# Kernel tuning notes

Measured on AMD Instinct MI355X. Metric: run time of the kernel, lower is better.

The kernel has to match this reference:

```python
import jax, jax.numpy as jnp
import numpy as np

B, S, D, H = 512, 256, 2, 256


def _lstm_cell(x, h, c, W_ih, W_hh, b_ih, b_hh):
    # PyTorch gate order: i, f, g, o
    gates = x @ W_ih.T + b_ih + h @ W_hh.T + b_hh
    i, f, g, o = jnp.split(gates, 4, axis=-1)
    c_new = jax.nn.sigmoid(f) * c + jax.nn.sigmoid(i) * jnp.tanh(g)
    h_new = jax.nn.sigmoid(o) * jnp.tanh(c_new)
    return h_new, c_new


def setup_inputs() -> dict:
    key = jax.random.key(0)
    ks = jax.random.split(key, 9)
    bound = 1.0 / np.sqrt(H)
    u = lambda k, shp: jax.random.uniform(k, shp, jnp.float32, -bound, bound)
    return {
        "inputs": jax.random.normal(ks[0], (B, S, D), jnp.float32),
        "enc_W_ih": u(ks[1], (4 * H, D)),
        "enc_W_hh": u(ks[2], (4 * H, H)),
        "enc_b_ih": u(ks[3], (4 * H,)),
        "enc_b_hh": u(ks[4], (4 * H,)),
        "dec_W_ih": u(ks[5], (4 * H, H)),
        "dec_W_hh": u(ks[6], (4 * H, H)),
        "dec_b_ih": u(ks[7], (4 * H,)),
        "dec_b_hh": u(ks[8], (4 * H,)),
    }


def reference(inputs, enc_W_ih, enc_W_hh, enc_b_ih, enc_b_hh,
              dec_W_ih, dec_W_hh, dec_b_ih, dec_b_hh):
    bsz, seq_len, _ = inputs.shape
    hid = enc_W_hh.shape[1]

    # ---- encoder LSTM (batch_first), h0 = c0 = 0 ----
    h0 = jnp.zeros((bsz, hid), inputs.dtype)
    c0 = jnp.zeros((bsz, hid), inputs.dtype)

    def enc_step(carry, x_t):
        h, c = carry
        h, c = _lstm_cell(x_t, h, c, enc_W_ih, enc_W_hh, enc_b_ih, enc_b_hh)
        return (h, c), h

    (h_last, c_last), enc_out_t = jax.lax.scan(enc_step, (h0, c0), inputs.transpose(1, 0, 2))
    enc_out = enc_out_t.transpose(1, 0, 2)  # [B, S, H]

    key = jax.random.key(42)
    keys = jax.random.split(key, seq_len)
    dec_in0 = jnp.zeros((bsz, hid), inputs.dtype)
    mask0 = jnp.zeros((bsz, seq_len), dtype=bool)
    rows = jnp.arange(bsz)

    def dec_step(carry, k):
        dec_in, h, c, mask = carry
        h, c = _lstm_cell(dec_in, h, c, dec_W_ih, dec_W_hh, dec_b_ih, dec_b_hh)
        scores = jnp.einsum('bsh,bh->bs', enc_out, h)          # bmm attention
        scores = jnp.where(mask, -jnp.inf, scores)             # mask visited
        idx = jax.random.categorical(k, scores, axis=1)        # multinomial(softmax)
        mask = mask.at[rows, idx].set(True)
        dec_in = jnp.take_along_axis(enc_out, idx[:, None, None], axis=1)[:, 0, :]
        return (dec_in, h, c, mask), idx

    _, indices_t = jax.lax.scan(dec_step, (dec_in0, h_last, c_last, mask0), keys)
    return indices_t.T  # [B, S] int
```

## Files before the change

### kernel.cpp

```cpp
#include <hip/hip_runtime.h>
#include <cstdint>
#include <cstddef>


typedef float v4f __attribute__((ext_vector_type(4)));
typedef unsigned long long u64;

#define WS_HX_OFF     0u
#define WS_AMX_OFF    (1u << 20)
#define WS_SYNC_BYTES 0x110000u
#define WS_ENCW4_OFF  (2u << 20)
#define WS_DECWI4_OFF (3u << 20)
#define WS_DECWH4_OFF (4u << 20)
#define WS_ENCK4_OFF  (5u << 20)
#define WS_NEEDED     ((size_t)(5u << 20) + (size_t)512 * 64 * 256 * 16)

__device__ __forceinline__ unsigned rotl32(unsigned x, int r) {
  return (x << r) | (x >> (32 - r));
}
__device__ __forceinline__ float sigm(float x) { return 1.f / (1.f + expf(-x)); }

__device__ __forceinline__ u64 pk(unsigned tag, unsigned payload) {
  return ((u64)tag << 32) | (u64)payload;
}
__device__ __forceinline__ unsigned spinrd(u64* p, unsigned tag) {
  u64 v = atomicAdd(p, 0ull);
  while ((unsigned)(v >> 32) != tag) {
    __builtin_amdgcn_s_sleep(2);
    v = atomicAdd(p, 0ull);
  }
  return (unsigned)v;
}

__device__ __forceinline__ void tf2(unsigned k0, unsigned k1,
                                    unsigned& x0, unsigned& x1) {
  const unsigned k2 = k0 ^ k1 ^ 0x1BD11BDAu;
  x0 += k0; x1 += k1;
  x0 += x1; x1 = rotl32(x1, 13); x1 ^= x0;
  x0 += x1; x1 = rotl32(x1, 15); x1 ^= x0;
  x0 += x1; x1 = rotl32(x1, 26); x1 ^= x0;
  x0 += x1; x1 = rotl32(x1,  6); x1 ^= x0;
  x0 += k1; x1 += k2 + 1u;
  x0 += x1; x1 = rotl32(x1, 17); x1 ^= x0;
  x0 += x1; x1 = rotl32(x1, 29); x1 ^= x0;
  x0 += x1; x1 = rotl32(x1, 16); x1 ^= x0;
  x0 += x1; x1 = rotl32(x1, 24); x1 ^= x0;
  x0 += k2; x1 += k0 + 2u;
  x0 += x1; x1 = rotl32(x1, 13); x1 ^= x0;
  x0 += x1; x1 = rotl32(x1, 15); x1 ^= x0;
  x0 += x1; x1 = rotl32(x1, 26); x1 ^= x0;
  x0 += x1; x1 = rotl32(x1,  6); x1 ^= x0;
  x0 += k0; x1 += k1 + 3u;
  x0 += x1; x1 = rotl32(x1, 17); x1 ^= x0;
  x0 += x1; x1 = rotl32(x1, 29); x1 ^= x0;
  x0 += x1; x1 = rotl32(x1, 16); x1 ^= x0;
  x0 += x1; x1 = rotl32(x1, 24); x1 ^= x0;
  x0 += k1; x1 += k2 + 4u;
  x0 += x1; x1 = rotl32(x1, 13); x1 ^= x0;
  x0 += x1; x1 = rotl32(x1, 15); x1 ^= x0;
  x0 += x1; x1 = rotl32(x1, 26); x1 ^= x0;
  x0 += x1; x1 = rotl32(x1,  6); x1 ^= x0;
  x0 += k2; x1 += k0 + 5u;
}

__global__ void repack_k(const float* __restrict__ eWh,
                         const float* __restrict__ dWi,
                         const float* __restrict__ dWh,
                         float* __restrict__ ws) {
  float* encW4 = (float*)((char*)ws + WS_ENCW4_OFF);
  float* decWi4 = (float*)((char*)ws + WS_DECWI4_OFF);
  float* decWh4 = (float*)((char*)ws + WS_DECWH4_OFF);
  const int n = blockIdx.x * blockDim.x + threadIdx.x;
  if (n >= 65536) return;
  const int k = n >> 8, u = n & 255;
#pragma unroll
  for (int g = 0; g < 4; ++g) {
    const int src = ((g << 8) + u) * 256 + k;
    const int dst = (n << 2) + g;
    encW4[dst] = eWh[src];
    decWi4[dst] = dWi[src];
    decWh4[dst] = dWh[src];
  }
}

__global__ void __launch_bounds__(1024)
ptrnet_kernel(const float* __restrict__ inp,
              const float* __restrict__ eWi,
              const float* __restrict__ eBi, const float* __restrict__ eBh,
              const float* __restrict__ dBi, const float* __restrict__ dBh,
              int* __restrict__ out,
              float* __restrict__ ws) {
  const int tid  = threadIdx.x;
  const int wave = tid >> 6, l = tid & 63;
  const int kq   = wave >> 2;
  const int uw   = wave & 3;
  const int uP   = (uw << 6) | l;
  const int k4b  = kq << 4;
  const int bA   = tid >> 8;
  const int uA   = tid & 255;

  const int g    = blockIdx.x & 127;
  const int H    = blockIdx.x >> 7;
  const int b0   = g << 2;
  const int bG   = b0 + bA;
  const int ubase = H << 7;
  const int pbase = ubase ^ 128;
  const int sbase = H << 7;

  const v4f* encW4  = (const v4f*)((char*)ws + WS_ENCW4_OFF);
  const v4f* decWi4 = (const v4f*)((char*)ws + WS_DECWI4_OFF);
  const v4f* decWh4 = (const v4f*)((char*)ws + WS_DECWH4_OFF);
  v4f* encK4 = (v4f*)((char*)ws + WS_ENCK4_OFF);

  u64* hxAll  = (u64*)((char*)ws + WS_HX_OFF);
  u64* hxMe   = hxAll + (size_t)g * 1024 + (size_t)H * 512;
  u64* hxYo   = hxAll + (size_t)g * 1024 + (size_t)(1 - H) * 512;
  u64* amxAll = (u64*)((char*)ws + WS_AMX_OFF);
  u64* amxMe  = amxAll + (size_t)g * 16 + (size_t)H * 8;
  u64* amxYo  = amxAll + (size_t)g * 16 + (size_t)(1 - H) * 8;

  __shared__ __align__(16) float hsF[2][1024];
  __shared__ __align__(16) v4f dinV[256];
  __shared__ __align__(16) v4f red[17][256];
  __shared__ unsigned char maskC[4][128];
  __shared__ float partV[4][2];
  __shared__ int   partI[4][2];
  __shared__ float oVs[4]; __shared__ int oIs[4];
  __shared__ float eVs[4]; __shared__ int eIs[4];

  const float ebi_ = eBi[uA] + eBh[uA];
  const float ebf_ = eBi[256 + uA] + eBh[256 + uA];
  const float ebg_ = eBi[512 + uA] + eBh[512 + uA];
  const float ebo_ = eBi[768 + uA] + eBh[768 + uA];
  const float wxi0 = eWi[2 * uA], wxi1 = eWi[2 * uA + 1];
  const float wxf0 = eWi[2 * (256 + uA)], wxf1 = eWi[2 * (256 + uA) + 1];
  const float wxg0 = eWi[2 * (512 + uA)], wxg1 = eWi[2 * (512 + uA) + 1];
  const float wxo0 = eWi[2 * (768 + uA)], wxo1 = eWi[2 * (768 + uA) + 1];

  hsF[0][tid] = 0.f;
  __syncthreads();

  float c = 0.f;
  int p = 0;

  for (int t = 0; t < 256; ++t) {
    v4f a0 = (v4f)0.f, a1 = (v4f)0.f, a2 = (v4f)0.f, a3 = (v4f)0.f;
    const v4f* Wp = encW4 + uP;
    const v4f* hq = (const v4f*)&hsF[p][0];
#pragma unroll 2
    for (int kk = 0; kk < 16; ++kk) {
      const int k4 = k4b + kk;
      const v4f w0 = Wp[(k4 * 4 + 0) << 8];
      const v4f w1 = Wp[(k4 * 4 + 1) << 8];
      const v4f w2 = Wp[(k4 * 4 + 2) << 8];
      const v4f w3 = Wp[(k4 * 4 + 3) << 8];
      const v4f h0 = hq[k4];
      const v4f h1 = hq[64 + k4];
      const v4f h2 = hq[128 + k4];
      const v4f h3 = hq[192 + k4];
      a0 += w0 * h0.x + w1 * h0.y + w2 * h0.z + w3 * h0.w;
      a1 += w0 * h1.x + w1 * h1.y + w2 * h1.z + w3 * h1.w;
      a2 += w0 * h2.x + w1 * h2.y + w2 * h2.z + w3 * h2.w;
      a3 += w0 * h3.x + w1 * h3.y + w2 * h3.z + w3 * h3.w;
    }
    red[(kq << 2) | 0][uP] = a0;
    red[(kq << 2) | 1][uP] = a1;
    red[(kq << 2) | 2][uP] = a2;
    red[(kq << 2) | 3][uP] = a3;
    __syncthreads();
    const v4f gv = red[bA][uA] + red[4 + bA][uA] + red[8 + bA][uA] + red[12 + bA][uA];
    const float2 xv = *(const float2*)(inp + (((bG) << 8) + t) * 2);
    const float ai = gv.x + ebi_ + wxi0 * xv.x + wxi1 * xv.y;
    const float af = gv.y + ebf_ + wxf0 * xv.x + wxf1 * xv.y;
    const float ag = gv.z + ebg_ + wxg0 * xv.x + wxg1 * xv.y;
    const float ao = gv.w + ebo_ + wxo0 * xv.x + wxo1 * xv.y;
    const float iv = sigm(ai), fv = sigm(af), gva = tanhf(ag), ov = sigm(ao);
    c = fv * c + iv * gva;
    const float hn = ov * tanhf(c);
    hsF[p ^ 1][(bA << 8) | uA] = hn;
    ((float*)encK4)[(((bG << 6) + (uA >> 2)) << 10) + (t << 2) + (uA & 3)] = hn;
    __syncthreads();
    p ^= 1;
  }

  float* creg = (float*)&red[0][0];
  creg[(bA << 8) | uA] = c;
  const int isP2 = tid < 512;
  const int bD = tid >> 7;
  const int uL = tid & 127;
  const int uD = ubase | uL;
  __syncthreads();
  float cD = 0.f, dbi2 = 0.f, dbf2 = 0.f, dbg2 = 0.f, dbo2 = 0.f;
  if (isP2) {
    cD = creg[(bD << 8) | uD];
    dbi2 = dBi[uD] + dBh[uD];
    dbf2 = dBi[256 + uD] + dBh[256 + uD];
    dbg2 = dBi[512 + uD] + dBh[512 + uD];
    dbo2 = dBi[768 + uD] + dBh[768 + uD];
  }
  const int aw  = wave - 8;
  const int bAt = aw >> 1;
  const int sL  = ((aw & 1) << 6) | l;
  const int sG  = sbase | sL;
  const int bGt = b0 + bAt;
  if (wave >= 8) maskC[bAt][sL] = 0;
  const int kqD  = wave >> 1;
  const int k4bD = kqD << 4;
  const int uPD  = ubase | ((wave & 1) << 6) | l;
  const float NEG_INF = __int_as_float((int)0xff800000);
  __syncthreads();

  {
    v4f a0 = (v4f)0.f, a1 = (v4f)0.f, a2 = (v4f)0.f, a3 = (v4f)0.f;
    const v4f* Wh = decWh4 + uP;
    const v4f* hq = (const v4f*)&hsF[p][0];
#pragma unroll 2
    for (int kk = 0; kk < 16; ++kk) {
      const int k4 = k4b + kk;
      const v4f w0 = Wh[(k4 * 4 + 0) << 8];
      const v4f w1 = Wh[(k4 * 4 + 1) << 8];
      const v4f w2 = Wh[(k4 * 4 + 2) << 8];
      const v4f w3 = Wh[(k4 * 4 + 3) << 8];
      const v4f h0 = hq[k4];
      const v4f h1 = hq[64 + k4];
      const v4f h2 = hq[128 + k4];
      const v4f h3 = hq[192 + k4];
      a0 += w0 * h0.x + w1 * h0.y + w2 * h0.z + w3 * h0.w;
      a1 += w0 * h1.x + w1 * h1.y + w2 * h1.z + w3 * h1.w;
      a2 += w0 * h2.x + w1 * h2.y + w2 * h2.z + w3 * h2.w;
      a3 += w0 * h3.x + w1 * h3.y + w2 * h3.z + w3 * h3.w;
    }
    red[(kq << 2) | 0][uP] = a0;
    red[(kq << 2) | 1][uP] = a1;
    red[(kq << 2) | 2][uP] = a2;
    red[(kq << 2) | 3][uP] = a3;
    __syncthreads();
    if (isP2) {
      const v4f gv = red[bD][uD] + red[4 + bD][uD] + red[8 + bD][uD] + red[12 + bD][uD];
      const float iv = sigm(gv.x + dbi2), fv = sigm(gv.y + dbf2);
      const float gva = tanhf(gv.z + dbg2), ov = sigm(gv.w + dbo2);
      cD = fv * cD + iv * gva;
      const float hn = ov * tanhf(cD);
      hsF[p ^ 1][(bD << 8) | uD] = hn;
      atomicExch(&hxMe[(bD << 7) | uL], pk(0xA5000000u, __float_as_uint(hn)));
      const unsigned pw = spinrd(&hxYo[(bD << 7) | uL], 0xA5000000u);
      hsF[p ^ 1][(bD << 8) | pbase | uL] = __uint_as_float(pw);
    }
    __syncthreads();
    p ^= 1;
  }

#define WINNER(B, WI) { float _wv = oVs[B]; int _wi = oIs[B];                 \
    const float _ev = eVs[B]; const int _ei = eIs[B];                         \
    if (_ev > _wv || (_ev == _wv && _ei < _wi)) { _wi = _ei; }                \
    WI = _wi; }

  for (int t = 0; t < 256; ++t) {
    const unsigned tagA = 0xA5000001u + 2u * (unsigned)t;
    const unsigned tagH = 0xA5000002u + 2u * (unsigned)t;
    const v4f* hq = (const v4f*)&hsF[p][0];

    if (wave < 8) {
      v4f a0 = (v4f)0.f, a1 = (v4f)0.f, a2 = (v4f)0.f, a3 = (v4f)0.f;
      const v4f* Wh = decWh4 + uPD;
#pragma unroll 2
      for (int kk = 0; kk < 16; ++kk) {
        const int k4 = k4bD + kk;
        const v4f w0 = Wh[(k4 * 4 + 0) << 8];
        const v4f w1 = Wh[(k4 * 4 + 1) << 8];
        const v4f w2 = Wh[(k4 * 4 + 2) << 8];
        const v4f w3 = Wh[(k4 * 4 + 3) << 8];
        const v4f h0 = hq[k4];
        const v4f h1 = hq[64 + k4];
        const v4f h2 = hq[128 + k4];
        const v4f h3 = hq[192 + k4];
        a0 += w0 * h0.x + w1 * h0.y + w2 * h0.z + w3 * h0.w;
        a1 += w0 * h1.x + w1 * h1.y + w2 * h1.z + w3 * h1.w;
        a2 += w0 * h2.x + w1 * h2.y + w2 * h2.z + w3 * h2.w;
        a3 += w0 * h3.x + w1 * h3.y + w2 * h3.z + w3 * h3.w;
      }
      red[(kqD << 2) | 0][uPD] = a0;
      red[(kqD << 2) | 1][uPD] = a1;
      red[(kqD << 2) | 2][uPD] = a2;
      red[(kqD << 2) | 3][uPD] = a3;
    } else {
      const int masked = maskC[bAt][sL];
      float sc = 0.f;
      if (!masked) {
        const v4f* E = encK4 + (bGt << 14) + sG;
        const v4f* hq2 = hq + (bAt << 6);
#pragma unroll 4
        for (int k4 = 0; k4 < 64; ++k4) {
          const v4f ev = E[k4 << 8];
          const v4f hv = hq2[k4];
          sc += ev.x * hv.x + ev.y * hv.y + ev.z * hv.z + ev.w * hv.w;
        }
      }
      unsigned bits;
      {
        unsigned kk0 = 0u, kk1 = (unsigned)t;
        tf2(0u, 42u, kk0, kk1);
        unsigned y0 = 0u, y1 = (unsigned)((bGt << 8) + sG);
        tf2(kk0, kk1, y0, y1);
        bits = y0 ^ y1;
      }
      const float fr = __uint_as_float((bits >> 9) | 0x3f800000u) - 1.0f;
      const float uu = (fr > 0.f) ? fr : 1.17549435e-38f;
      const float gum = -logf(-logf(uu));
      float bv = masked ? NEG_INF : (sc + gum);
      int bi = sG;
#pragma unroll
      for (int off = 32; off; off >>= 1) {
        const float ov2 = __shfl_xor(bv, off, 64);
        const int oi2 = __shfl_xor(bi, off, 64);
        if (ov2 > bv || (ov2 == bv && oi2 < bi)) { bv = ov2; bi = oi2; }
      }
      if (l == 0) { partV[bAt][aw & 1] = bv; partI[bAt][aw & 1] = bi; }
    }
    __syncthreads();

    if (tid < 4) {
      float v0 = partV[tid][0]; int i0 = partI[tid][0];
      const float v1 = partV[tid][1];
      if (v1 > v0) { v0 = v1; i0 = partI[tid][1]; }
      oVs[tid] = v0; oIs[tid] = i0;
      atomicExch(&amxMe[tid * 2 + 0], pk(tagA, __float_as_uint(v0)));
      atomicExch(&amxMe[tid * 2 + 1], pk(tagA, (unsigned)i0));
    }
    if (tid >= 64 && tid < 72) {
      const int j = tid - 64;
      const unsigned pw = spinrd(&amxYo[j], tagA);
      if (j & 1) eIs[j >> 1] = (int)pw;
      else       eVs[j >> 1] = __uint_as_float(pw);
    }
    __syncthreads();

    if (wave >= 8) {
      int wi; WINNER(bAt, wi);
      if (sG == wi) maskC[bAt][sL] = 1;
    }
    if (H == 0 && tid < 4) {
      int wi; WINNER(tid, wi);
      out[((b0 + tid) << 8) + t] = wi;
    }
    if (tid < 256) {
      const int bb = tid >> 6, k4s = tid & 63;
      int wi; WINNER(bb, wi);
      dinV[tid] = encK4[((((b0 + bb) << 6) | k4s) << 8) + wi];
    }
    __syncthreads();

    if (t == 255) break;

    if (wave < 8) {
      v4f a0 = red[(kqD << 2) | 0][uPD];
      v4f a1 = red[(kqD << 2) | 1][uPD];
      v4f a2 = red[(kqD << 2) | 2][uPD];
      v4f a3 = red[(kqD << 2) | 3][uPD];
      const v4f* Wi = decWi4 + uPD;
#pragma unroll 2
      for (int kk = 0; kk < 16; ++kk) {
        const int k4 = k4bD + kk;
        const v4f w0 = Wi[(k4 * 4 + 0) << 8];
        const v4f w1 = Wi[(k4 * 4 + 1) << 8];
        const v4f w2 = Wi[(k4 * 4 + 2) << 8];
        const v4f w3 = Wi[(k4 * 4 + 3) << 8];
        const v4f d0 = dinV[k4];
        const v4f d1 = dinV[64 + k4];
        const v4f d2 = dinV[128 + k4];
        const v4f d3 = dinV[192 + k4];
        a0 += w0 * d0.x + w1 * d0.y + w2 * d0.z + w3 * d0.w;
        a1 += w0 * d1.x + w1 * d1.y + w2 * d1.z + w3 * d1.w;
        a2 += w0 * d2.x + w1 * d2.y + w2 * d2.z + w3 * d2.w;
        a3 += w0 * d3.x + w1 * d3.y + w2 * d3.z + w3 * d3.w;
      }
      red[(kqD << 2) | 0][uPD] = a0;
      red[(kqD << 2) | 1][uPD] = a1;
      red[(kqD << 2) | 2][uPD] = a2;
      red[(kqD << 2) | 3][uPD] = a3;
    }
    __syncthreads();

    if (isP2) {
      const v4f gv = red[bD][uD] + red[4 + bD][uD] + red[8 + bD][uD] + red[12 + bD][uD];
      const float iv = sigm(gv.x + dbi2), fv = sigm(gv.y + dbf2);
      const float gva = tanhf(gv.z + dbg2), ov = sigm(gv.w + dbo2);
      cD = fv * cD + iv * gva;
      const float hn = ov * tanhf(cD);
      hsF[p ^ 1][(bD << 8) | uD] = hn;
      atomicExch(&hxMe[(bD << 7) | uL], pk(tagH, __float_as_uint(hn)));
      const unsigned pw = spinrd(&hxYo[(bD << 7) | uL], tagH);
      hsF[p ^ 1][(bD << 8) | pbase | uL] = __uint_as_float(pw);
    }
    __syncthreads();
    p ^= 1;
  }
#undef WINNER
}

extern "C" void kernel_launch(void* const* d_in, const int* in_sizes, int n_in,
                              void* d_out, int out_size, void* d_ws, size_t ws_size,
                              hipStream_t stream) {
  (void)in_sizes; (void)n_in; (void)out_size;
  if (ws_size < WS_NEEDED) return;

  const float* inp = (const float*)d_in[0];
  const float* eWi = (const float*)d_in[1];
  const float* eWh = (const float*)d_in[2];
  const float* eBi = (const float*)d_in[3];
  const float* eBh = (const float*)d_in[4];
  const float* dWi = (const float*)d_in[5];
  const float* dWh = (const float*)d_in[6];
  const float* dBi = (const float*)d_in[7];
  const float* dBh = (const float*)d_in[8];
  int* out = (int*)d_out;
  float* wsf = (float*)d_ws;

  hipMemsetAsync((char*)d_ws + WS_HX_OFF, 0, WS_SYNC_BYTES, stream);
  hipLaunchKernelGGL(repack_k, dim3(256), dim3(256), 0, stream, eWh, dWi, dWh, wsf);
  hipLaunchKernelGGL(ptrnet_kernel, dim3(256), dim3(1024), 0, stream,
                     inp, eWi, eBi, eBh, dBi, dBh, out, wsf);
}
```

Before: 9.274 ms.

## Split encoder LSTM gate matvec across block pair with cross-block exchange

Each block pair previously computed the full encoder recurrence redundantly. Now each block of the pair handles two of the four gates (repacked as v2f weights), halving per-block weight reads. Gate partial sums and new hidden halves are exchanged with the partner block through global-memory tagged atomics and a spin flag every timestep. This adds two cross-block synchronisations per step on the serial encoder path.

```diff
diff --git a/kernel.cpp b/kernel.cpp
--- a/kernel.cpp
+++ b/kernel.cpp
@@ -4,16 +4,19 @@
 
 
 typedef float v4f __attribute__((ext_vector_type(4)));
+typedef float v2f __attribute__((ext_vector_type(2)));
 typedef unsigned long long u64;
 
-#define WS_HX_OFF     0u
-#define WS_AMX_OFF    (1u << 20)
-#define WS_SYNC_BYTES 0x110000u
-#define WS_ENCW4_OFF  (2u << 20)
-#define WS_DECWI4_OFF (3u << 20)
-#define WS_DECWH4_OFF (4u << 20)
-#define WS_ENCK4_OFF  (5u << 20)
-#define WS_NEEDED     ((size_t)(5u << 20) + (size_t)512 * 64 * 256 * 16)
+#define WS_HX_OFF     0x000000u
+#define WS_GX_OFF     0x100000u
+#define WS_AMX_OFF    0x200000u
+#define WS_GFLAG_OFF  0x204000u
+#define WS_SYNC_BYTES 0x205000u
+#define WS_ENCW2_OFF  0x300000u
+#define WS_DECWI4_OFF 0x400000u
+#define WS_DECWH4_OFF 0x500000u
+#define WS_ENCK4_OFF  0x600000u
+#define WS_NEEDED     ((size_t)WS_ENCK4_OFF + (size_t)512 * 64 * 256 * 16)
 
 __device__ __forceinline__ unsigned rotl32(unsigned x, int r) {
   return (x << r) | (x >> (32 - r));
@@ -67,7 +70,7 @@
                          const float* __restrict__ dWi,
                          const float* __restrict__ dWh,
                          float* __restrict__ ws) {
-  float* encW4 = (float*)((char*)ws + WS_ENCW4_OFF);
+  float* encW2 = (float*)((char*)ws + WS_ENCW2_OFF);
   float* decWi4 = (float*)((char*)ws + WS_DECWI4_OFF);
   float* decWh4 = (float*)((char*)ws + WS_DECWH4_OFF);
   const int n = blockIdx.x * blockDim.x + threadIdx.x;
@@ -76,10 +79,9 @@
 #pragma unroll
   for (int g = 0; g < 4; ++g) {
     const int src = ((g << 8) + u) * 256 + k;
-    const int dst = (n << 2) + g;
-    encW4[dst] = eWh[src];
-    decWi4[dst] = dWi[src];
-    decWh4[dst] = dWh[src];
+    decWi4[(n << 2) + g] = dWi[src];
+    decWh4[(n << 2) + g] = dWh[src];
+    encW2[(((g >> 1) << 16) + n) * 2 + (g & 1)] = eWh[src];
   }
 }
 
@@ -96,18 +98,21 @@
   const int uw   = wave & 3;
   const int uP   = (uw << 6) | l;
   const int k4b  = kq << 4;
-  const int bA   = tid >> 8;
-  const int uA   = tid & 255;
 
   const int g    = blockIdx.x & 127;
   const int H    = blockIdx.x >> 7;
   const int b0   = g << 2;
-  const int bG   = b0 + bA;
   const int ubase = H << 7;
   const int pbase = ubase ^ 128;
   const int sbase = H << 7;
 
-  const v4f* encW4  = (const v4f*)((char*)ws + WS_ENCW4_OFF);
+  const int isP2 = tid < 512;
+  const int bD = tid >> 7;
+  const int uL = tid & 127;
+  const int uD = ubase | uL;
+  const int bGD = b0 + bD;
+
+  const v2f* encW2o = (const v2f*)((char*)ws + WS_ENCW2_OFF) + (H << 16);
   const v4f* decWi4 = (const v4f*)((char*)ws + WS_DECWI4_OFF);
   const v4f* decWh4 = (const v4f*)((char*)ws + WS_DECWH4_OFF);
   v4f* encK4 = (v4f*)((char*)ws + WS_ENCK4_OFF);
@@ -115,9 +120,15 @@
   u64* hxAll  = (u64*)((char*)ws + WS_HX_OFF);
   u64* hxMe   = hxAll + (size_t)g * 1024 + (size_t)H * 512;
   u64* hxYo   = hxAll + (size_t)g * 1024 + (size_t)(1 - H) * 512;
+  u64* gxAll  = (u64*)((char*)ws + WS_GX_OFF);
+  u64* gxMe   = gxAll + (size_t)g * 1024 + (size_t)H * 512;
+  u64* gxYo   = gxAll + (size_t)g * 1024 + (size_t)(1 - H) * 512;
   u64* amxAll = (u64*)((char*)ws + WS_AMX_OFF);
   u64* amxMe  = amxAll + (size_t)g * 16 + (size_t)H * 8;
   u64* amxYo  = amxAll + (size_t)g * 16 + (size_t)(1 - H) * 8;
+  u64* gfAll  = (u64*)((char*)ws + WS_GFLAG_OFF);
+  u64* gflagMe = gfAll + (size_t)g * 2 + (size_t)H;
+  u64* gflagYo = gfAll + (size_t)g * 2 + (size_t)(1 - H);
 
   __shared__ __align__(16) float hsF[2][1024];
   __shared__ __align__(16) v4f dinV[256];
@@ -127,72 +138,100 @@
   __shared__ int   partI[4][2];
   __shared__ float oVs[4]; __shared__ int oIs[4];
   __shared__ float eVs[4]; __shared__ int eIs[4];
-
-  const float ebi_ = eBi[uA] + eBh[uA];
-  const float ebf_ = eBi[256 + uA] + eBh[256 + uA];
-  const float ebg_ = eBi[512 + uA] + eBh[512 + uA];
-  const float ebo_ = eBi[768 + uA] + eBh[768 + uA];
-  const float wxi0 = eWi[2 * uA], wxi1 = eWi[2 * uA + 1];
-  const float wxf0 = eWi[2 * (256 + uA)], wxf1 = eWi[2 * (256 + uA) + 1];
-  const float wxg0 = eWi[2 * (512 + uA)], wxg1 = eWi[2 * (512 + uA) + 1];
-  const float wxo0 = eWi[2 * (768 + uA)], wxo1 = eWi[2 * (768 + uA) + 1];
+  v2f* red2 = (v2f*)&red[0][0];
+
+  const int uB = isP2 ? uD : 0;
+  const float ebi_ = eBi[uB] + eBh[uB];
+  const float ebf_ = eBi[256 + uB] + eBh[256 + uB];
+  const float ebg_ = eBi[512 + uB] + eBh[512 + uB];
+  const float ebo_ = eBi[768 + uB] + eBh[768 + uB];
+  const float wxi0 = eWi[2 * uB], wxi1 = eWi[2 * uB + 1];
+  const float wxf0 = eWi[2 * (256 + uB)], wxf1 = eWi[2 * (256 + uB) + 1];
+  const float wxg0 = eWi[2 * (512 + uB)], wxg1 = eWi[2 * (512 + uB) + 1];
+  const float wxo0 = eWi[2 * (768 + uB)], wxo1 = eWi[2 * (768 + uB) + 1];
 
   hsF[0][tid] = 0.f;
   __syncthreads();
 
-  float c = 0.f;
+  float cD = 0.f;
   int p = 0;
 
   for (int t = 0; t < 256; ++t) {
-    v4f a0 = (v4f)0.f, a1 = (v4f)0.f, a2 = (v4f)0.f, a3 = (v4f)0.f;
-    const v4f* Wp = encW4 + uP;
-    const v4f* hq = (const v4f*)&hsF[p][0];
+    {
+      v2f a0 = (v2f)0.f, a1 = (v2f)0.f, a2 = (v2f)0.f, a3 = (v2f)0.f;
+      const v2f* Wp = encW2o + uP;
+      const v4f* hq = (const v4f*)&hsF[p][0];
 #pragma unroll 2
-    for (int kk = 0; kk < 16; ++kk) {
-      const int k4 = k4b + kk;
-      const v4f w0 = Wp[(k4 * 4 + 0) << 8];
-      const v4f w1 = Wp[(k4 * 4 + 1) << 8];
-      const v4f w2 = Wp[(k4 * 4 + 2) << 8];
-      const v4f w3 = Wp[(k4 * 4 + 3) << 8];
-      const v4f h0 = hq[k4];
-      const v4f h1 = hq[64 + k4];
-      const v4f h2 = hq[128 + k4];
-      const v4f h3 = hq[192 + k4];
-      a0 += w0 * h0.x + w1 * h0.y + w2 * h0.z + w3 * h0.w;
-      a1 += w0 * h1.x + w1 * h1.y + w2 * h1.z + w3 * h1.w;
-      a2 += w0 * h2.x + w1 * h2.y + w2 * h2.z + w3 * h2.w;
-      a3 += w0 * h3.x + w1 * h3.y + w2 * h3.z + w3 * h3.w;
-    }
-    red[(kq << 2) | 0][uP] = a0;
-    red[(kq << 2) | 1][uP] = a1;
-    red[(kq << 2) | 2][uP] = a2;
-    red[(kq << 2) | 3][uP] = a3;
-    __syncthreads();
-    const v4f gv = red[bA][uA] + red[4 + bA][uA] + red[8 + bA][uA] + red[12 + bA][uA];
-    const float2 xv = *(const float2*)(inp + (((bG) << 8) + t) * 2);
-    const float ai = gv.x + ebi_ + wxi0 * xv.x + wxi1 * xv.y;
-    const float af = gv.y + ebf_ + wxf0 * xv.x + wxf1 * xv.y;
-    const float ag = gv.z + ebg_ + wxg0 * xv.x + wxg1 * xv.y;
-    const float ao = gv.w + ebo_ + wxo0 * xv.x + wxo1 * xv.y;
-    const float iv = sigm(ai), fv = sigm(af), gva = tanhf(ag), ov = sigm(ao);
-    c = fv * c + iv * gva;
-    const float hn = ov * tanhf(c);
-    hsF[p ^ 1][(bA << 8) | uA] = hn;
-    ((float*)encK4)[(((bG << 6) + (uA >> 2)) << 10) + (t << 2) + (uA & 3)] = hn;
+      for (int kk = 0; kk < 16; ++kk) {
+        const int k4 = k4b + kk;
+        const v2f w0 = Wp[(k4 * 4 + 0) << 8];
+        const v2f w1 = Wp[(k4 * 4 + 1) << 8];
+        const v2f w2 = Wp[(k4 * 4 + 2) << 8];
+        const v2f w3 = Wp[(k4 * 4 + 3) << 8];
+        const v4f h0 = hq[k4];
+        const v4f h1 = hq[64 + k4];
+        const v4f h2 = hq[128 + k4];
+        const v4f h3 = hq[192 + k4];
+        a0 += w0 * h0.x + w1 * h0.y + w2 * h0.z + w3 * h0.w;
+        a1 += w0 * h1.x + w1 * h1.y + w2 * h1.z + w3 * h1.w;
+        a2 += w0 * h2.x + w1 * h2.y + w2 * h2.z + w3 * h2.w;
+        a3 += w0 * h3.x + w1 * h3.y + w2 * h3.z + w3 * h3.w;
+      }
+      red2[(((kq << 2) | 0) << 8) + uP] = a0;
+      red2[(((kq << 2) | 1) << 8) + uP] = a1;
+      red2[(((kq << 2) | 2) << 8) + uP] = a2;
+      red2[(((kq << 2) | 3) << 8) + uP] = a3;
+    }
+    __syncthreads();
+
+    if (isP2) {
+      const int upub = pbase | uL;
+      v2f gx = red2[(bD << 8) + upub];
+      gx += red2[((4 + bD) << 8) + upub];
+      gx += red2[((8 + bD) << 8) + upub];
+      gx += red2[((12 + bD) << 8) + upub];
+      const u64 pkd = ((u64)__float_as_uint(gx.y) << 32) | (u64)__float_as_uint(gx.x);
+      atomicExch(&gxMe[(bD << 7) | uL], pkd);
+    }
+    __syncthreads();
+    if (tid == 0) {
+      atomicExch(gflagMe, pk(0xB0000001u + (unsigned)t, 0u));
+      (void)spinrd(gflagYo, 0xB0000001u + (unsigned)t);
+    }
+    __syncthreads();
+
+    if (isP2) {
+      v2f own = red2[(bD << 8) + uD];
+      own += red2[((4 + bD) << 8) + uD];
+      own += red2[((8 + bD) << 8) + uD];
+      own += red2[((12 + bD) << 8) + uD];
+      const u64 pw = atomicAdd(&gxYo[(bD << 7) | uL], 0ull);
+      const float ox = __uint_as_float((unsigned)pw);
+      const float oy = __uint_as_float((unsigned)(pw >> 32));
+      const float gvI = H ? ox : own.x;
+      const float gvF = H ? oy : own.y;
+      const float gvG = H ? own.x : ox;
+      const float gvO = H ? own.y : oy;
+      const float2 xv = *(const float2*)(inp + (((bGD) << 8) + t) * 2);
+      const float ai = gvI + ebi_ + wxi0 * xv.x + wxi1 * xv.y;
+      const float af = gvF + ebf_ + wxf0 * xv.x + wxf1 * xv.y;
+      const float ag = gvG + ebg_ + wxg0 * xv.x + wxg1 * xv.y;
+      const float ao = gvO + ebo_ + wxo0 * xv.x + wxo1 * xv.y;
+      const float iv = sigm(ai), fv = sigm(af), gva = tanhf(ag), ov = sigm(ao);
+      cD = fv * cD + iv * gva;
+      const float hn = ov * tanhf(cD);
+      hsF[p ^ 1][(bD << 8) | uD] = hn;
+      ((float*)encK4)[(((bGD << 6) + (uD >> 2)) << 10) + (t << 2) + (uD & 3)] = hn;
+      atomicExch(&hxMe[(bD << 7) | uL], pk(0xC0000001u + (unsigned)t, __float_as_uint(hn)));
+      const unsigned pw2 = spinrd(&hxYo[(bD << 7) | uL], 0xC0000001u + (unsigned)t);
+      hsF[p ^ 1][(bD << 8) | pbase | uL] = __uint_as_float(pw2);
+    }
     __syncthreads();
     p ^= 1;
   }
 
-  float* creg = (float*)&red[0][0];
-  creg[(bA << 8) | uA] = c;
-  const int isP2 = tid < 512;
-  const int bD = tid >> 7;
-  const int uL = tid & 127;
-  const int uD = ubase | uL;
-  __syncthreads();
-  float cD = 0.f, dbi2 = 0.f, dbf2 = 0.f, dbg2 = 0.f, dbo2 = 0.f;
+  float dbi2 = 0.f, dbf2 = 0.f, dbg2 = 0.f, dbo2 = 0.f;
   if (isP2) {
-    cD = creg[(bD << 8) | uD];
     dbi2 = dBi[uD] + dBh[uD];
     dbf2 = dBi[256 + uD] + dBh[256 + uD];
     dbg2 = dBi[512 + uD] + dBh[512 + uD];
@@ -416,7 +455,7 @@
   int* out = (int*)d_out;
   float* wsf = (float*)d_ws;
 
-  hipMemsetAsync((char*)d_ws + WS_HX_OFF, 0, WS_SYNC_BYTES, stream);
+  hipMemsetAsync((char*)d_ws, 0, WS_SYNC_BYTES, stream);
   hipLaunchKernelGGL(repack_k, dim3(256), dim3(256), 0, stream, eWh, dWi, dWh, wsf);
   hipLaunchKernelGGL(ptrnet_kernel, dim3(256), dim3(1024), 0, stream,
                      inp, eWi, eBi, eBh, dBi, dBh, out, wsf);
```

New measurement: 9.350 ms. About the same (+0.8%).

## Spread decoder input-projection across all waves and publish per-wave argmax partials directly

Applied to the files above, without the earlier changes.

The decoder's W_ih·dec_in matvec, previously run only by waves 0-7 with float4 weight loads, is split across all 16 waves, each handling half of the gate components with float2 loads. This halves per-wave latency on the serial critical path. The cross-block argmax exchange now packs value, index and tag into a single 64-bit word per wave partial and publishes it right after the wave reduction, so the extra barrier before publishing is gone. The consumer merges two remote partials per batch row. Packing the index into 8 bits and the tag into 24 bits limits the encodable range.

```diff
diff --git a/kernel.cpp b/kernel.cpp
--- a/kernel.cpp
+++ b/kernel.cpp
@@ -4,6 +4,7 @@
 
 
 typedef float v4f __attribute__((ext_vector_type(4)));
+typedef float v2f __attribute__((ext_vector_type(2)));
 typedef unsigned long long u64;
 
 #define WS_HX_OFF     0u
@@ -23,6 +24,9 @@
 __device__ __forceinline__ u64 pk(unsigned tag, unsigned payload) {
   return ((u64)tag << 32) | (u64)payload;
 }
+__device__ __forceinline__ u64 pk49(unsigned tag9, float v, int idx) {
+  return ((u64)tag9 << 40) | ((u64)__float_as_uint(v) << 8) | (u64)(idx & 0xFF);
+}
 __device__ __forceinline__ unsigned spinrd(u64* p, unsigned tag) {
   u64 v = atomicAdd(p, 0ull);
   while ((unsigned)(v >> 32) != tag) {
@@ -30,6 +34,14 @@
     v = atomicAdd(p, 0ull);
   }
   return (unsigned)v;
+}
+__device__ __forceinline__ u64 spinrd49(u64* p, unsigned tag9) {
+  u64 v = atomicAdd(p, 0ull);
+  while ((unsigned)(v >> 40) != tag9) {
+    __builtin_amdgcn_s_sleep(2);
+    v = atomicAdd(p, 0ull);
+  }
+  return v;
 }
 
 __device__ __forceinline__ void tf2(unsigned k0, unsigned k1,
@@ -126,7 +138,7 @@
   __shared__ float partV[4][2];
   __shared__ int   partI[4][2];
   __shared__ float oVs[4]; __shared__ int oIs[4];
-  __shared__ float eVs[4]; __shared__ int eIs[4];
+  __shared__ float eV2[4][2]; __shared__ int eI2[4][2];
 
   const float ebi_ = eBi[uA] + eBh[uA];
   const float ebf_ = eBi[256 + uA] + eBh[256 + uA];
@@ -207,6 +219,10 @@
   const int kqD  = wave >> 1;
   const int k4bD = kqD << 4;
   const int uPD  = ubase | ((wave & 1) << 6) | l;
+  const int kqW  = wave >> 2;
+  const int k4bW = kqW << 4;
+  const int gp   = (wave >> 1) & 1;
+  const int uW   = ubase | ((wave & 1) << 6) | l;
   const float NEG_INF = __int_as_float((int)0xff800000);
   __syncthreads();
 
@@ -251,12 +267,14 @@
   }
 
 #define WINNER(B, WI) { float _wv = oVs[B]; int _wi = oIs[B];                 \
-    const float _ev = eVs[B]; const int _ei = eIs[B];                         \
-    if (_ev > _wv || (_ev == _wv && _ei < _wi)) { _wi = _ei; }                \
+    { const float _e = eV2[B][0]; const int _i = eI2[B][0];                   \
+      if (_e > _wv || (_e == _wv && _i < _wi)) { _wv = _e; _wi = _i; } }      \
+    { const float _e = eV2[B][1]; const int _i = eI2[B][1];                   \
+      if (_e > _wv || (_e == _wv && _i < _wi)) { _wv = _e; _wi = _i; } }      \
     WI = _wi; }
 
   for (int t = 0; t < 256; ++t) {
-    const unsigned tagA = 0xA5000001u + 2u * (unsigned)t;
+    const unsigned tagA9 = (unsigned)t + 1u;
     const unsigned tagH = 0xA5000002u + 2u * (unsigned)t;
     const v4f* hq = (const v4f*)&hsF[p][0];
 
@@ -315,7 +333,10 @@
         const int oi2 = __shfl_xor(bi, off, 64);
         if (ov2 > bv || (ov2 == bv && oi2 < bi)) { bv = ov2; bi = oi2; }
       }
-      if (l == 0) { partV[bAt][aw & 1] = bv; partI[bAt][aw & 1] = bi; }
+      if (l == 0) {
+        partV[bAt][aw & 1] = bv; partI[bAt][aw & 1] = bi;
+        atomicExch(&amxMe[(bAt << 1) | (aw & 1)], pk49(tagA9, bv, bi));
+      }
     }
     __syncthreads();
 
@@ -324,14 +345,12 @@
       const float v1 = partV[tid][1];
       if (v1 > v0) { v0 = v1; i0 = partI[tid][1]; }
       oVs[tid] = v0; oIs[tid] = i0;
-      atomicExch(&amxMe[tid * 2 + 0], pk(tagA, __float_as_uint(v0)));
-      atomicExch(&amxMe[tid * 2 + 1], pk(tagA, (unsigned)i0));
     }
     if (tid >= 64 && tid < 72) {
       const int j = tid - 64;
-      const unsigned pw = spinrd(&amxYo[j], tagA);
-      if (j & 1) eIs[j >> 1] = (int)pw;
-      else       eVs[j >> 1] = __uint_as_float(pw);
+      const u64 w = spinrd49(&amxYo[j], tagA9);
+      eV2[j >> 1][j & 1] = __uint_as_float((unsigned)(w >> 8));
+      eI2[j >> 1][j & 1] = (int)(w & 0xFF);
     }
     __syncthreads();
 
@@ -352,19 +371,22 @@
 
     if (t == 255) break;
 
-    if (wave < 8) {
-      v4f a0 = red[(kqD << 2) | 0][uPD];
-      v4f a1 = red[(kqD << 2) | 1][uPD];
-      v4f a2 = red[(kqD << 2) | 2][uPD];
-      v4f a3 = red[(kqD << 2) | 3][uPD];
-      const v4f* Wi = decWi4 + uPD;
+    {
+      const float* redb = (const float*)&red[0][0];
+      float* redw = (float*)&red[0][0];
+      const int uo = (uW << 2) | (gp << 1);
+      v2f a0 = *(const v2f*)(redb + (((kqW << 2) | 0) << 10) + uo);
+      v2f a1 = *(const v2f*)(redb + (((kqW << 2) | 1) << 10) + uo);
+      v2f a2 = *(const v2f*)(redb + (((kqW << 2) | 2) << 10) + uo);
+      v2f a3 = *(const v2f*)(redb + (((kqW << 2) | 3) << 10) + uo);
+      const float* Wib = (const float*)decWi4;
 #pragma unroll 2
       for (int kk = 0; kk < 16; ++kk) {
-        const int k4 = k4bD + kk;
-        const v4f w0 = Wi[(k4 * 4 + 0) << 8];
-        const v4f w1 = Wi[(k4 * 4 + 1) << 8];
-        const v4f w2 = Wi[(k4 * 4 + 2) << 8];
-        const v4f w3 = Wi[(k4 * 4 + 3) << 8];
+        const int k4 = k4bW + kk;
+        const v2f w0 = *(const v2f*)(Wib + (((k4 * 4 + 0) << 8) << 2) + uo);
+        const v2f w1 = *(const v2f*)(Wib + (((k4 * 4 + 1) << 8) << 2) + uo);
+        const v2f w2 = *(const v2f*)(Wib + (((k4 * 4 + 2) << 8) << 2) + uo);
+        const v2f w3 = *(const v2f*)(Wib + (((k4 * 4 + 3) << 8) << 2) + uo);
         const v4f d0 = dinV[k4];
         const v4f d1 = dinV[64 + k4];
         const v4f d2 = dinV[128 + k4];
@@ -374,10 +396,10 @@
         a2 += w0 * d2.x + w1 * d2.y + w2 * d2.z + w3 * d2.w;
         a3 += w0 * d3.x + w1 * d3.y + w2 * d3.z + w3 * d3.w;
       }
-      red[(kqD << 2) | 0][uPD] = a0;
-      red[(kqD << 2) | 1][uPD] = a1;
-      red[(kqD << 2) | 2][uPD] = a2;
-      red[(kqD << 2) | 3][uPD] = a3;
+      *(v2f*)(redw + (((kqW << 2) | 0) << 10) + uo) = a0;
+      *(v2f*)(redw + (((kqW << 2) | 1) << 10) + uo) = a1;
+      *(v2f*)(redw + (((kqW << 2) | 2) << 10) + uo) = a2;
+      *(v2f*)(redw + (((kqW << 2) | 3) << 10) + uo) = a3;
     }
     __syncthreads();
 
```

After: 9.498 ms. 1.02x slower.
